# Kernel optimization log

Hardware: AMD Instinct MI355X
Metric: run time of the kernel (lower is better)

The kernel has to match this reference:

```python
import jax, jax.numpy as jnp
import numpy as np

N_SEG, B, COND = 16, 256, 512
H, OUT = 1024, 512


def setup_inputs() -> dict:
    key = jax.random.key(0)
    ks = jax.random.split(key, 14)
    s = 0.05  # keep gates in non-saturated range
    return {
        "c": jax.random.normal(ks[0], (N_SEG, B, COND), jnp.float32),
        "W_init": jax.random.normal(ks[1], (4 * H, COND), jnp.float32) * s,
        "b_init": jax.random.normal(ks[2], (4 * H,), jnp.float32) * s,
        "W_ih1": jax.random.normal(ks[3], (4 * H, COND + OUT), jnp.float32) * s,
        "W_hh1": jax.random.normal(ks[4], (4 * H, H), jnp.float32) * s,
        "b_ih1": jax.random.normal(ks[5], (4 * H,), jnp.float32) * s,
        "b_hh1": jax.random.normal(ks[6], (4 * H,), jnp.float32) * s,
        "W_ih2": jax.random.normal(ks[7], (4 * H, H), jnp.float32) * s,
        "W_hh2": jax.random.normal(ks[8], (4 * H, H), jnp.float32) * s,
        "b_ih2": jax.random.normal(ks[9], (4 * H,), jnp.float32) * s,
        "b_hh2": jax.random.normal(ks[10], (4 * H,), jnp.float32) * s,
        "W_out": jax.random.normal(ks[11], (OUT, H), jnp.float32) * s,
        "b_out": jax.random.normal(ks[12], (OUT,), jnp.float32) * s,
        "length": 32,
        "epoch": 10,
        "k": 200,
    }


def _lstm_cell(x, h, c, W_ih, W_hh, b_ih, b_hh):
    # PyTorch LSTMCell gate order: input, forget, cell, output
    g = x @ W_ih.T + b_ih + h @ W_hh.T + b_hh
    i, f, gg, o = jnp.split(g, 4, axis=-1)
    c_new = jax.nn.sigmoid(f) * c + jax.nn.sigmoid(i) * jnp.tanh(gg)
    h_new = jax.nn.sigmoid(o) * jnp.tanh(c_new)
    return h_new, c_new


def reference(c, W_init, b_init, W_ih1, W_hh1, b_ih1, b_hh1,
              W_ih2, W_hh2, b_ih2, b_hh2, W_out, b_out,
              length, epoch, k):
    steps = length // 2
    n_seg, bsz, _ = c.shape

    def segment(prev, embed):
        # fresh LSTM states from the conductor embedding
        t = jnp.tanh(embed @ W_init.T + b_init)  # [B, 4H]
        h1, h2, c1, c2 = jnp.split(t, 4, axis=-1)

        def step(carry, _):
            h1, c1, h2, c2, prev = carry
            prev = jax.lax.stop_gradient(prev)  # training=False path: detach
            x = jnp.concatenate([embed, prev], axis=1)  # [B, COND+OUT]
            h1n, c1n = _lstm_cell(x, h1, c1, W_ih1, W_hh1, b_ih1, b_hh1)
            h2n, c2n = _lstm_cell(h1n, h2, c2, W_ih2, W_hh2, b_ih2, b_hh2)
            out = h2n @ W_out.T + b_out  # [B, OUT]
            return (h1n, c1n, h2n, c2n, out), out

        (_, _, _, _, prev), outs = jax.lax.scan(
            step, (h1, h2_init := h2, c1, c2, prev)[:0] or (h1, c1, h2, c2, prev),
            None, length=steps)
        return prev, outs  # outs: [steps, B, OUT]

    prev0 = jnp.zeros((bsz, OUT), dtype=c.dtype)
    _, outs = jax.lax.scan(segment, prev0, c)  # [n_seg, steps, B, OUT]
    outputs = outs.reshape(n_seg * steps, bsz, OUT).transpose(1, 0, 2)
    ratio = jnp.float32(k / (k + np.exp(epoch / k)))
    return outputs, ratio
```

## Files before the change

kernel.cpp:

```cpp
#include <hip/hip_runtime.h>
#include <hip/hip_bf16.h>

using bf16 = __hip_bfloat16;
typedef __attribute__((ext_vector_type(8))) short bf16x8;
typedef __attribute__((ext_vector_type(4))) float f32x4;

__device__ __forceinline__ void gload16(const void* g, void* l) {
  __builtin_amdgcn_global_load_lds((const __attribute__((address_space(1))) void*)g,
                                   (__attribute__((address_space(3))) void*)l, 16, 0, 0);
}

__device__ __forceinline__ float sigm(float x) { return 1.0f / (1.0f + __expf(-x)); }
__device__ __forceinline__ float ftanh(float x) {
  float e = __expf(2.0f * fabsf(x));
  return copysignf(1.0f - 2.0f / (e + 1.0f), x);
}

#define MFMA16(a, b, c) __builtin_amdgcn_mfma_f32_16x16x32_bf16(a, b, c, 0, 0, 0)
#define WAITV2() asm volatile("s_waitcnt vmcnt(2)" ::: "memory")
#define WAITV0() asm volatile("s_waitcnt vmcnt(0)" ::: "memory")
#define BARRIER() do { __builtin_amdgcn_s_barrier(); asm volatile("" ::: "memory"); } while (0)

struct Frag { bf16x8 a0, a1, b0, b1; };

__global__ __launch_bounds__(512) void rnn_step(
    const bf16* __restrict__ a1, const bf16* __restrict__ a2,
    const bf16* __restrict__ w1, const bf16* __restrict__ w2,
    const float* __restrict__ pe, const float* __restrict__ bias,
    const float* __restrict__ bsub,
    const float* __restrict__ c_in, float* __restrict__ c_out,
    bf16* __restrict__ h_out)
{
  __shared__ __attribute__((aligned(128))) char smem[65536];
  const int tid = threadIdx.x;
  const int wv = tid >> 6, ln = tid & 63;
  const int grp = wv >> 2, wg = wv & 3;
  const int bid = blockIdx.x;
  const int nt = ((bid & 7) << 3) | ((bid >> 3) & 7);
  const int mt = bid >> 6;
  const int m0 = mt << 6, n0 = nt << 6;
  const int wm = (wg >> 1) << 5, wn = (wg & 1) << 5;
  const bool use2 = (a2 != nullptr);

  const bf16* asrc = (grp == 0) ? a1 : (use2 ? a2 : a1);
  const bf16* wsrc = (grp == 0) ? w1 : (use2 ? w2 : w1);
  char* gbase = smem + (grp << 15);

  const int srow = (wg << 4) + (ln >> 2);
  const int skc  = (ln & 3) ^ ((srow >> 1) & 3);
  const size_t aGOff = ((size_t)(m0 + srow) << 11) + (skc << 4);
  const size_t bGOff = ((size_t)(n0 + srow) << 11) + (skc << 4);

  auto stage = [&](int kb) {
    char* dst = gbase + ((kb & 3) << 13) + (wg << 10);
    gload16((const char*)asrc + aGOff + ((size_t)kb << 6), dst);
    gload16((const char*)wsrc + bGOff + ((size_t)kb << 6), dst + 4096);
  };

  const int kc = ln >> 4;
  const int ar0 = wm + (ln & 15), ar1 = ar0 + 16;
  const int br0 = wn + (ln & 15), br1 = br0 + 16;
  const int aoff0 = ar0 * 64 + ((kc ^ ((ar0 >> 1) & 3)) << 4);
  const int aoff1 = ar1 * 64 + ((kc ^ ((ar1 >> 1) & 3)) << 4);
  const int boff0 = 4096 + br0 * 64 + ((kc ^ ((br0 >> 1) & 3)) << 4);
  const int boff1 = 4096 + br1 * 64 + ((kc ^ ((br1 >> 1) & 3)) << 4);

  auto ldfrags = [&](int kb, Frag& f) {
    const char* base = gbase + ((kb & 3) << 13);
    f.a0 = *(const bf16x8*)(base + aoff0);
    f.a1 = *(const bf16x8*)(base + aoff1);
    f.b0 = *(const bf16x8*)(base + boff0);
    f.b1 = *(const bf16x8*)(base + boff1);
  };

  f32x4 acc00{}, acc01{}, acc10{}, acc11{};
  auto domfma = [&](Frag& f) {
    acc00 = MFMA16(f.a0, f.b0, acc00);
    acc01 = MFMA16(f.a0, f.b1, acc01);
    acc10 = MFMA16(f.a1, f.b0, acc10);
    acc11 = MFMA16(f.a1, f.b1, acc11);
  };

  Frag f0, f1;
  stage(0); stage(1);
  WAITV2(); BARRIER();
  stage(2);
  ldfrags(0, f0);
  __builtin_amdgcn_s_setprio(1);
  for (int kb = 1; kb < 31; kb += 2) {
    WAITV2(); BARRIER();
    stage(kb + 2);
    ldfrags(kb, f1);
    domfma(f0);
    WAITV2(); BARRIER();
    if (kb + 3 < 32) stage(kb + 3);
    ldfrags(kb + 1, f0);
    domfma(f1);
  }
  WAITV0(); BARRIER();
  ldfrags(31, f1);
  domfma(f0);
  domfma(f1);
  __builtin_amdgcn_s_setprio(0);

  __syncthreads();
  float* gs = (float*)smem;
#pragma unroll
  for (int mi = 0; mi < 2; ++mi)
#pragma unroll
    for (int ni = 0; ni < 2; ++ni) {
      f32x4 a = (mi == 0) ? (ni == 0 ? acc00 : acc01) : (ni == 0 ? acc10 : acc11);
#pragma unroll
      for (int r = 0; r < 4; ++r) {
        int row = wm + mi * 16 + ((ln >> 4) << 2) + r;
        int col = wn + ni * 16 + (ln & 15);
        gs[grp * 4352 + row * 68 + col] = a[r];
      }
    }
  __syncthreads();

  const int h = tid & 15, mr = tid >> 4;
  const int hg = (nt << 4) + h;
#pragma unroll
  for (int half = 0; half < 2; ++half) {
    int m = mr + (half << 5);
    int gm = m0 + m;
    float4 v = *(const float4*)(gs + m * 68 + (h << 2));
    float g0 = v.x, g1 = v.y, g2 = v.z, g3 = v.w;
    if (use2) {
      float4 u = *(const float4*)(gs + 4352 + m * 68 + (h << 2));
      g0 += u.x; g1 += u.y; g2 += u.z; g3 += u.w;
    }
    int nb = n0 + (h << 2);
    if (pe) { float4 pv = *(const float4*)(pe + (size_t)gm * 4096 + nb);
              g0 += pv.x; g1 += pv.y; g2 += pv.z; g3 += pv.w; }
    if (bias){ float4 bv = *(const float4*)(bias + nb);
              g0 += bv.x; g1 += bv.y; g2 += bv.z; g3 += bv.w; }
    if (bsub){ float4 sv = *(const float4*)(bsub + nb);
              g0 -= sv.x; g1 -= sv.y; g2 -= sv.z; g3 -= sv.w; }
    float ig = sigm(g0), fg = sigm(g1), gg = ftanh(g2), og = sigm(g3);
    size_t idx = (size_t)gm * 1024 + hg;
    float cn = fg * c_in[idx] + ig * gg;
    c_out[idx] = cn;
    h_out[idx] = __float2bfloat16(og * ftanh(cn));
  }
}

template <int EP>
__global__ __launch_bounds__(256) void gemm_ep(
    const bf16* __restrict__ A, const bf16* __restrict__ W, int K,
    const float* __restrict__ bias,
    float* __restrict__ f1, float* __restrict__ f2,
    bf16* __restrict__ o1, bf16* __restrict__ o2, int gt_base)
{
  __shared__ __attribute__((aligned(128))) char smem[32768];
  const int tid = threadIdx.x;
  const int wv = tid >> 6, ln = tid & 63;
  const int n0 = blockIdx.x << 6;
  const int m0 = blockIdx.y << 6;
  const int Nn = (int)(gridDim.x << 6);
  const int wm = (wv >> 1) << 5, wn = (wv & 1) << 5;
  const int nkb = K >> 6;

  f32x4 acc00{}, acc01{}, acc10{}, acc11{};

  auto stage = [&](int kb, int buf) {
    int k0 = kb << 6;
    char* As = smem + buf * 16384;
    char* Bs = As + 8192;
#pragma unroll
    for (int i = 0; i < 2; ++i) {
      int r = ((i << 2) + wv) * 8 + (ln >> 3);
      int sc = (ln & 7) ^ (r & 7);
      gload16((const char*)(A + (size_t)(m0 + r) * K + k0) + (sc << 4),
              As + (((i << 2) + wv) << 10));
      gload16((const char*)(W + (size_t)(n0 + r) * K + k0) + (sc << 4),
              Bs + (((i << 2) + wv) << 10));
    }
  };

  stage(0, 0);
  __syncthreads();
  for (int kb = 0; kb < nkb; ++kb) {
    int buf = kb & 1;
    if (kb + 1 < nkb) stage(kb + 1, buf ^ 1);
    const char* As = smem + buf * 16384;
    const char* Bs = As + 8192;
#pragma unroll
    for (int ks = 0; ks < 2; ++ks) {
      const int kc = (ks << 2) + (ln >> 4);
      auto ld = [&](const char* base, int row) -> bf16x8 {
        return *(const bf16x8*)(base + row * 128 + ((kc ^ (row & 7)) << 4));
      };
      bf16x8 A0 = ld(As, wm + (ln & 15));
      bf16x8 A1 = ld(As, wm + 16 + (ln & 15));
      bf16x8 B0 = ld(Bs, wn + (ln & 15));
      bf16x8 B1 = ld(Bs, wn + 16 + (ln & 15));
      acc00 = MFMA16(A0, B0, acc00);
      acc01 = MFMA16(A0, B1, acc01);
      acc10 = MFMA16(A1, B0, acc10);
      acc11 = MFMA16(A1, B1, acc11);
    }
    __syncthreads();
  }

#pragma unroll
  for (int mi = 0; mi < 2; ++mi)
#pragma unroll
    for (int ni = 0; ni < 2; ++ni) {
      f32x4 a = (mi == 0) ? (ni == 0 ? acc00 : acc01) : (ni == 0 ? acc10 : acc11);
#pragma unroll
      for (int r = 0; r < 4; ++r) {
        int m = m0 + wm + mi * 16 + ((ln >> 4) << 2) + r;
        int n = n0 + wn + ni * 16 + (ln & 15);
        float v = a[r];
        if constexpr (EP == 0) {
          o1[(size_t)m * Nn + n] = __float2bfloat16(v);
        } else if constexpr (EP == 1) {
          v = tanhf(v + bias[n]);
          int q = n >> 10, hh = n & 1023;
          size_t idx = (size_t)m * 1024 + hh;
          if (q == 0)      o1[idx] = __float2bfloat16(v);
          else if (q == 1) o2[idx] = __float2bfloat16(v);
          else if (q == 2) f1[idx] = v;
          else             f2[idx] = v;
        } else if constexpr (EP == 2) {
          f1[(size_t)m * 4096 + n] = v + bias[n];
        } else {
          int b = m & 255, g = (m >> 8) + gt_base;
          f1[(size_t)b * 131072 + (size_t)g * 512 + n] = v + bias[n];
        }
      }
    }
}

__global__ void k_conv(const float* __restrict__ s, bf16* __restrict__ d, int n) {
  int i = blockIdx.x * 256 + threadIdx.x;
  if (i < n) d[i] = __float2bfloat16(s[i]);
}
__global__ void k_trans_wout(const float* __restrict__ s, bf16* __restrict__ d) {
  int i = blockIdx.x * 256 + threadIdx.x;
  int l = i >> 9, j = i & 511;
  d[i] = __float2bfloat16(s[(size_t)j * 1024 + l]);
}
__global__ void k_reorder_g(const float* __restrict__ s, bf16* __restrict__ d) {
  int i = blockIdx.x * 256 + threadIdx.x;
  int np = i >> 10, kx = i & 1023;
  int hh = np >> 2, q = np & 3;
  d[i] = __float2bfloat16(s[(size_t)(q * 1024 + hh) * 1024 + kx]);
}
__global__ void k_reorder_c(const float* __restrict__ s, bf16* __restrict__ d, int coloff) {
  int i = blockIdx.x * 256 + threadIdx.x;
  int np = i >> 9, kx = i & 511;
  int hh = np >> 2, q = np & 3;
  d[i] = __float2bfloat16(s[(size_t)(q * 1024 + hh) * 1024 + coloff + kx]);
}
__global__ void k_bias(const float* __restrict__ bih1, const float* __restrict__ bhh1,
                       const float* __restrict__ bih2, const float* __restrict__ bhh2,
                       const float* __restrict__ bo,   const float* __restrict__ Wih1,
                       float* __restrict__ b1r, float* __restrict__ b2r,
                       float* __restrict__ bfr) {
  int n = blockIdx.x * 256 + threadIdx.x;
  int hh = n >> 2, q = n & 3, r = q * 1024 + hh;
  const float* wrow = Wih1 + (size_t)r * 1024 + 512;
  float acc = 0.f;
  for (int j = 0; j < 512; ++j) acc += bo[j] * wrow[j];
  bfr[n] = acc;
  b1r[n] = bih1[r] + bhh1[r] + acc;
  b2r[n] = bih2[r] + bhh2[r];
}
__global__ void k_ratio(float* __restrict__ dst, const int* __restrict__ ep,
                        const int* __restrict__ kv) {
  float kf = (float)kv[0];
  dst[0] = kf / (kf + __expf((float)ep[0] / kf));
}

extern "C" void kernel_launch(void* const* d_in, const int* in_sizes, int n_in,
                              void* d_out, int out_size, void* d_ws, size_t ws_size,
                              hipStream_t stream) {
  (void)in_sizes; (void)n_in;
  const float* in_c     = (const float*)d_in[0];
  const float* in_Winit = (const float*)d_in[1];
  const float* in_binit = (const float*)d_in[2];
  const float* in_Wih1  = (const float*)d_in[3];
  const float* in_Whh1  = (const float*)d_in[4];
  const float* in_bih1  = (const float*)d_in[5];
  const float* in_bhh1  = (const float*)d_in[6];
  const float* in_Wih2  = (const float*)d_in[7];
  const float* in_Whh2  = (const float*)d_in[8];
  const float* in_bih2  = (const float*)d_in[9];
  const float* in_bhh2  = (const float*)d_in[10];
  const float* in_Wout  = (const float*)d_in[11];
  const float* in_bout  = (const float*)d_in[12];
  const int*   in_epoch = (const int*)d_in[14];
  const int*   in_k     = (const int*)d_in[15];
  float* out = (float*)d_out;

  char* p = (char*)d_ws;
  auto alloc = [&](size_t bytes) { char* q = p; p += (bytes + 255) & ~(size_t)255; return q; };
  bf16* wHH1  = (bf16*)alloc(4096ull * 1024 * 2);
  bf16* wFOLD = (bf16*)alloc(4096ull * 1024 * 2);
  bf16* wIH2  = (bf16*)alloc(4096ull * 1024 * 2);
  bf16* wHH2  = (bf16*)alloc(4096ull * 1024 * 2);
  bf16* wOUT  = (bf16*)alloc(512ull * 1024 * 2);
  bf16* wOUTT = (bf16*)alloc(1024ull * 512 * 2);
  bf16* wINIT = (bf16*)alloc(4096ull * 512 * 2);
  bf16* wIH1C = (bf16*)alloc(4096ull * 512 * 2);
  bf16* wPREV = (bf16*)alloc(4096ull * 512 * 2);
  bf16* cbf   = (bf16*)alloc(4096ull * 512 * 2);
  float* b1r  = (float*)alloc(4096 * 4);
  float* b2r  = (float*)alloc(4096 * 4);
  float* bfr  = (float*)alloc(4096 * 4);
  bf16* h1i   = (bf16*)alloc(16ull * 256 * 1024 * 2);
  bf16* h2i   = (bf16*)alloc(16ull * 256 * 1024 * 2);
  float* c1i  = (float*)alloc(16ull * 256 * 1024 * 4);
  float* c2i  = (float*)alloc(16ull * 256 * 1024 * 4);
  float* PE1  = (float*)alloc(16ull * 256 * 4096 * 4);
  bf16* h1b[2]; float* c1b[2]; float* c2b[2]; bf16* h2b[2];
  for (int i = 0; i < 2; ++i) {
    h1b[i] = (bf16*)alloc(256ull * 1024 * 2);
    c1b[i] = (float*)alloc(256ull * 1024 * 4);
    c2b[i] = (float*)alloc(256ull * 1024 * 4);
    h2b[i] = (bf16*)alloc(256ull * 1024 * 2);
  }
  bf16* hist = (bf16*)alloc(256ull * 256 * 1024 * 2);
  size_t need_full = (size_t)(p - (char*)d_ws);
  bool primary = ws_size >= need_full;

  k_conv<<<8192, 256, 0, stream>>>(in_c, cbf, 2097152);
  k_conv<<<2048, 256, 0, stream>>>(in_Wout, wOUT, 524288);
  k_conv<<<8192, 256, 0, stream>>>(in_Winit, wINIT, 2097152);
  k_trans_wout<<<2048, 256, 0, stream>>>(in_Wout, wOUTT);
  k_reorder_g<<<16384, 256, 0, stream>>>(in_Whh1, wHH1);
  k_reorder_g<<<16384, 256, 0, stream>>>(in_Wih2, wIH2);
  k_reorder_g<<<16384, 256, 0, stream>>>(in_Whh2, wHH2);
  k_reorder_c<<<8192, 256, 0, stream>>>(in_Wih1, wIH1C, 0);
  k_reorder_c<<<8192, 256, 0, stream>>>(in_Wih1, wPREV, 512);
  k_bias<<<16, 256, 0, stream>>>(in_bih1, in_bhh1, in_bih2, in_bhh2, in_bout,
                                 in_Wih1, b1r, b2r, bfr);
  gemm_ep<0><<<dim3(16, 64), 256, 0, stream>>>(wPREV, wOUTT, 512, nullptr,
                                               nullptr, nullptr, wFOLD, nullptr, 0);
  gemm_ep<1><<<dim3(64, 64), 256, 0, stream>>>(cbf, wINIT, 512, in_binit,
                                               c1i, c2i, h1i, h2i, 0);
  gemm_ep<2><<<dim3(64, 64), 256, 0, stream>>>(cbf, wIH1C, 512, b1r,
                                               PE1, nullptr, nullptr, nullptr, 0);

  const size_t S = 256ull * 1024;
  for (int s = 0; s < 16; ++s) {
    for (int t = 0; t < 16; ++t) {
      int gt = s * 16 + t;
      int cur = gt & 1, prv = cur ^ 1;
      const bf16* h2prev = (gt == 0) ? nullptr
                          : (primary ? hist + (size_t)(gt - 1) * S : h2b[prv]);
      rnn_step<<<256, 512, 0, stream>>>(
          (t == 0) ? h1i + (size_t)s * S : h1b[prv], h2prev,
          wHH1, wFOLD,
          PE1 + (size_t)s * 1048576, nullptr, (gt == 0) ? bfr : nullptr,
          (t == 0) ? c1i + (size_t)s * S : c1b[prv], c1b[cur], h1b[cur]);
      rnn_step<<<256, 512, 0, stream>>>(
          h1b[cur],
          (t == 0) ? h2i + (size_t)s * S
                   : (primary ? hist + (size_t)(gt - 1) * S : h2b[prv]),
          wIH2, wHH2, nullptr, b2r, nullptr,
          (t == 0) ? c2i + (size_t)s * S : c2b[prv], c2b[cur],
          primary ? hist + (size_t)gt * S : h2b[cur]);
      if (!primary) {
        gemm_ep<3><<<dim3(8, 4), 256, 0, stream>>>(h2b[cur], wOUT, 1024, in_bout,
                                                   out, nullptr, nullptr, nullptr, gt);
      }
    }
  }

  if (primary) {
    gemm_ep<3><<<dim3(8, 1024), 256, 0, stream>>>(hist, wOUT, 1024, in_bout,
                                                  out, nullptr, nullptr, nullptr, 0);
  }
  k_ratio<<<1, 1, 0, stream>>>(out + (out_size - 1), in_epoch, in_k);
}
```

Baseline: 6.608 ms.

## Deepen LDS prefetch pipeline to eight stages with paired k-block consumption

Result: faster. 6.141 ms (-7.1%).

```diff
diff --git a/kernel.cpp b/kernel.cpp
--- a/kernel.cpp
+++ b/kernel.cpp
@@ -17,8 +17,7 @@
 }
 
 #define MFMA16(a, b, c) __builtin_amdgcn_mfma_f32_16x16x32_bf16(a, b, c, 0, 0, 0)
-#define WAITV2() asm volatile("s_waitcnt vmcnt(2)" ::: "memory")
-#define WAITV0() asm volatile("s_waitcnt vmcnt(0)" ::: "memory")
+#define WAITV(n) asm volatile("s_waitcnt vmcnt(" #n ")" ::: "memory")
 #define BARRIER() do { __builtin_amdgcn_s_barrier(); asm volatile("" ::: "memory"); } while (0)
 
 struct Frag { bf16x8 a0, a1, b0, b1; };
@@ -31,7 +30,7 @@
     const float* __restrict__ c_in, float* __restrict__ c_out,
     bf16* __restrict__ h_out)
 {
-  __shared__ __attribute__((aligned(128))) char smem[65536];
+  __shared__ __attribute__((aligned(128))) char smem[131072];
   const int tid = threadIdx.x;
   const int wv = tid >> 6, ln = tid & 63;
   const int grp = wv >> 2, wg = wv & 3;
@@ -44,7 +43,7 @@
 
   const bf16* asrc = (grp == 0) ? a1 : (use2 ? a2 : a1);
   const bf16* wsrc = (grp == 0) ? w1 : (use2 ? w2 : w1);
-  char* gbase = smem + (grp << 15);
+  char* gbase = smem + (grp << 16);
 
   const int srow = (wg << 4) + (ln >> 2);
   const int skc  = (ln & 3) ^ ((srow >> 1) & 3);
@@ -52,7 +51,7 @@
   const size_t bGOff = ((size_t)(n0 + srow) << 11) + (skc << 4);
 
   auto stage = [&](int kb) {
-    char* dst = gbase + ((kb & 3) << 13) + (wg << 10);
+    char* dst = gbase + ((kb & 7) << 13) + (wg << 10);
     gload16((const char*)asrc + aGOff + ((size_t)kb << 6), dst);
     gload16((const char*)wsrc + bGOff + ((size_t)kb << 6), dst + 4096);
   };
@@ -66,7 +65,7 @@
   const int boff1 = 4096 + br1 * 64 + ((kc ^ ((br1 >> 1) & 3)) << 4);
 
   auto ldfrags = [&](int kb, Frag& f) {
-    const char* base = gbase + ((kb & 3) << 13);
+    const char* base = gbase + ((kb & 7) << 13);
     f.a0 = *(const bf16x8*)(base + aoff0);
     f.a1 = *(const bf16x8*)(base + aoff1);
     f.b0 = *(const bf16x8*)(base + boff0);
@@ -82,25 +81,32 @@
   };
 
   Frag f0, f1;
-  stage(0); stage(1);
-  WAITV2(); BARRIER();
-  stage(2);
-  ldfrags(0, f0);
+  stage(0); stage(1); stage(2); stage(3); stage(4); stage(5);
+  WAITV(8); BARRIER();
+  ldfrags(0, f0); ldfrags(1, f1);
+  stage(6); stage(7);
   __builtin_amdgcn_s_setprio(1);
-  for (int kb = 1; kb < 31; kb += 2) {
-    WAITV2(); BARRIER();
-    stage(kb + 2);
-    ldfrags(kb, f1);
-    domfma(f0);
-    WAITV2(); BARRIER();
-    if (kb + 3 < 32) stage(kb + 3);
-    ldfrags(kb + 1, f0);
-    domfma(f1);
-  }
-  WAITV0(); BARRIER();
-  ldfrags(31, f1);
-  domfma(f0);
-  domfma(f1);
+  domfma(f0); domfma(f1);
+  __builtin_amdgcn_s_setprio(0);
+  for (int p = 1; p <= 13; ++p) {
+    const int kb = p << 1;
+    WAITV(8); BARRIER();
+    ldfrags(kb, f0); ldfrags(kb + 1, f1);
+    if (kb + 6 < 32) stage(kb + 6);
+    if (kb + 7 < 32) stage(kb + 7);
+    __builtin_amdgcn_s_setprio(1);
+    domfma(f0); domfma(f1);
+    __builtin_amdgcn_s_setprio(0);
+  }
+  WAITV(4); BARRIER();
+  ldfrags(28, f0); ldfrags(29, f1);
+  __builtin_amdgcn_s_setprio(1);
+  domfma(f0); domfma(f1);
+  __builtin_amdgcn_s_setprio(0);
+  WAITV(0); BARRIER();
+  ldfrags(30, f0); ldfrags(31, f1);
+  __builtin_amdgcn_s_setprio(1);
+  domfma(f0); domfma(f1);
   __builtin_amdgcn_s_setprio(0);
 
   __syncthreads();
```

## Load MFMA fragments directly from global memory with register prefetch, dropping LDS staging

Applied to the files above, without the earlier changes.

New measurement: 20.56 ms. +211.1%, slower.

```diff
diff --git a/kernel.cpp b/kernel.cpp
--- a/kernel.cpp
+++ b/kernel.cpp
@@ -17,9 +17,6 @@
 }
 
 #define MFMA16(a, b, c) __builtin_amdgcn_mfma_f32_16x16x32_bf16(a, b, c, 0, 0, 0)
-#define WAITV2() asm volatile("s_waitcnt vmcnt(2)" ::: "memory")
-#define WAITV0() asm volatile("s_waitcnt vmcnt(0)" ::: "memory")
-#define BARRIER() do { __builtin_amdgcn_s_barrier(); asm volatile("" ::: "memory"); } while (0)
 
 struct Frag { bf16x8 a0, a1, b0, b1; };
 
@@ -31,7 +28,7 @@
     const float* __restrict__ c_in, float* __restrict__ c_out,
     bf16* __restrict__ h_out)
 {
-  __shared__ __attribute__((aligned(128))) char smem[65536];
+  __shared__ __attribute__((aligned(128))) float gs[2 * 64 * 68];
   const int tid = threadIdx.x;
   const int wv = tid >> 6, ln = tid & 63;
   const int grp = wv >> 2, wg = wv & 3;
@@ -44,67 +41,38 @@
 
   const bf16* asrc = (grp == 0) ? a1 : (use2 ? a2 : a1);
   const bf16* wsrc = (grp == 0) ? w1 : (use2 ? w2 : w1);
-  char* gbase = smem + (grp << 15);
-
-  const int srow = (wg << 4) + (ln >> 2);
-  const int skc  = (ln & 3) ^ ((srow >> 1) & 3);
-  const size_t aGOff = ((size_t)(m0 + srow) << 11) + (skc << 4);
-  const size_t bGOff = ((size_t)(n0 + srow) << 11) + (skc << 4);
-
-  auto stage = [&](int kb) {
-    char* dst = gbase + ((kb & 3) << 13) + (wg << 10);
-    gload16((const char*)asrc + aGOff + ((size_t)kb << 6), dst);
-    gload16((const char*)wsrc + bGOff + ((size_t)kb << 6), dst + 4096);
-  };
-
-  const int kc = ln >> 4;
-  const int ar0 = wm + (ln & 15), ar1 = ar0 + 16;
-  const int br0 = wn + (ln & 15), br1 = br0 + 16;
-  const int aoff0 = ar0 * 64 + ((kc ^ ((ar0 >> 1) & 3)) << 4);
-  const int aoff1 = ar1 * 64 + ((kc ^ ((ar1 >> 1) & 3)) << 4);
-  const int boff0 = 4096 + br0 * 64 + ((kc ^ ((br0 >> 1) & 3)) << 4);
-  const int boff1 = 4096 + br1 * 64 + ((kc ^ ((br1 >> 1) & 3)) << 4);
-
-  auto ldfrags = [&](int kb, Frag& f) {
-    const char* base = gbase + ((kb & 3) << 13);
-    f.a0 = *(const bf16x8*)(base + aoff0);
-    f.a1 = *(const bf16x8*)(base + aoff1);
-    f.b0 = *(const bf16x8*)(base + boff0);
-    f.b1 = *(const bf16x8*)(base + boff1);
-  };
+
+  const int kc = ln >> 4, r15 = ln & 15;
+  const char* pa0 = (const char*)asrc + ((size_t)(m0 + wm + r15) << 11) + (kc << 4);
+  const char* pa1 = pa0 + (16 << 11);
+  const char* pb0 = (const char*)wsrc + ((size_t)(n0 + wn + r15) << 11) + (kc << 4);
+  const char* pb1 = pb0 + (16 << 11);
 
   f32x4 acc00{}, acc01{}, acc10{}, acc11{};
-  auto domfma = [&](Frag& f) {
+  auto domfma = [&](const Frag& f) {
     acc00 = MFMA16(f.a0, f.b0, acc00);
     acc01 = MFMA16(f.a0, f.b1, acc01);
     acc10 = MFMA16(f.a1, f.b0, acc10);
     acc11 = MFMA16(f.a1, f.b1, acc11);
   };
 
-  Frag f0, f1;
-  stage(0); stage(1);
-  WAITV2(); BARRIER();
-  stage(2);
-  ldfrags(0, f0);
-  __builtin_amdgcn_s_setprio(1);
-  for (int kb = 1; kb < 31; kb += 2) {
-    WAITV2(); BARRIER();
-    stage(kb + 2);
-    ldfrags(kb, f1);
-    domfma(f0);
-    WAITV2(); BARRIER();
-    if (kb + 3 < 32) stage(kb + 3);
-    ldfrags(kb + 1, f0);
-    domfma(f1);
-  }
-  WAITV0(); BARRIER();
-  ldfrags(31, f1);
-  domfma(f0);
-  domfma(f1);
-  __builtin_amdgcn_s_setprio(0);
-
-  __syncthreads();
-  float* gs = (float*)smem;
+#define LOADF(kb, f) do {                              \
+    (f).a0 = *(const bf16x8*)(pa0 + (kb) * 64);        \
+    (f).a1 = *(const bf16x8*)(pa1 + (kb) * 64);        \
+    (f).b0 = *(const bf16x8*)(pb0 + (kb) * 64);        \
+    (f).b1 = *(const bf16x8*)(pb1 + (kb) * 64);        \
+  } while (0)
+
+  Frag fr[6];
+#pragma unroll
+  for (int kb = 0; kb < 6; ++kb) LOADF(kb, fr[kb]);
+#pragma unroll
+  for (int kb = 0; kb < 32; ++kb) {
+    domfma(fr[kb % 6]);
+    if (kb + 6 < 32) LOADF(kb + 6, fr[kb % 6]);
+  }
+#undef LOADF
+
 #pragma unroll
   for (int mi = 0; mi < 2; ++mi)
 #pragma unroll
```
